# Performance work log

Hardware: AMD Instinct MI355X
Metric: run time of the kernel (lower is better)

The kernel has to match this reference:

```python
import jax, jax.numpy as jnp
import numpy as np

B, C, H, W, IC = 8, 128, 64, 32, 64
NEG = -9.0e15  # matches torch's -9000000000000000.0 mask value


def setup_inputs() -> dict:
    key = jax.random.key(0)
    ks = jax.random.split(key, 8)
    x = jax.random.normal(ks[0], (B, C, H, W), dtype=jnp.float32)
    adj = jax.random.randint(ks[1], (H * W, H * W), 0, 2, dtype=jnp.int32)
    s = 0.1  # keep pre-softmax logits in a sane range
    g_w = jax.random.normal(ks[2], (IC, C), dtype=jnp.float32) * s
    theta_w = jax.random.normal(ks[3], (IC, C), dtype=jnp.float32) * s
    phi_w = jax.random.normal(ks[4], (IC, C), dtype=jnp.float32) * s
    cp_w = jax.random.normal(ks[5], (2 * IC,), dtype=jnp.float32) * s
    g_b = jnp.zeros((IC,), jnp.float32)
    theta_b = jnp.zeros((IC,), jnp.float32)
    phi_b = jnp.zeros((IC,), jnp.float32)
    return {"x": x, "adj": adj, "g_w": g_w, "g_b": g_b, "theta_w": theta_w,
            "theta_b": theta_b, "phi_w": phi_w, "phi_b": phi_b, "cp_w": cp_w}


def reference(x, adj, g_w, g_b, theta_w, theta_b, phi_w, phi_b, cp_w):
    b, c, h, w = x.shape
    n = h * w
    ic = g_w.shape[0]
    xf = x.reshape(b, c, n)  # flatten spatial sites: (B,C,N)
    # 1x1 convs == per-site linear projections
    g_x = jnp.einsum('oc,bcn->bno', g_w, xf) + g_b          # (B,N,IC)
    th = jnp.einsum('oc,bcn->bon', theta_w, xf) + theta_b[:, None]  # (B,IC,N)
    ph = jnp.einsum('oc,bcn->bon', phi_w, xf) + phi_b[:, None]      # (B,IC,N)
    # concat_project 1x1 conv on [theta;phi] channels == broadcast sum of two dot products
    w_t, w_p = cp_w[:ic], cp_w[ic:]
    f_t = jnp.einsum('o,bon->bn', w_t, th)  # (B,N)
    f_p = jnp.einsum('o,bon->bn', w_p, ph)  # (B,N)
    e = jax.nn.leaky_relu(f_t[:, :, None] + f_p[:, None, :], 0.2)  # (B,N,N)
    attention = jnp.where(adj > 0, jnp.float32(NEG), e)
    attention = jax.nn.softmax(attention, axis=-1)
    y = jnp.einsum('bij,bjo->bio', attention, g_x)  # (B,N,IC)
    return y.transpose(0, 2, 1).reshape(b, ic, h, w)
```

## Files before the change

### kernel.cpp

```cpp
#include <hip/hip_runtime.h>
#include <hip/hip_bf16.h>
#include <cstdint>

#define B_   8
#define C_   128
#define IC_  64
#define N_   2048
#define NEGF (-9000000000000000.0f)
#define ROWS 16

typedef __attribute__((ext_vector_type(8))) short bf16x8;
typedef __attribute__((ext_vector_type(4))) float f32x4;

#define OFF_FT   0
#define OFF_FP   16384
#define OFF_VT   32768
#define OFF_VP   32896
#define OFF_VB   33024
#define OFF_GXB  33040

static __device__ __forceinline__ ushort f2bf(float f) {
  __hip_bfloat16 h = __float2bfloat16(f);
  return *reinterpret_cast<ushort*>(&h);
}

__global__ void k_prep(const float* __restrict__ theta_w,
                       const float* __restrict__ theta_b,
                       const float* __restrict__ phi_w,
                       const float* __restrict__ phi_b,
                       const float* __restrict__ cp_w,
                       float* __restrict__ ws) {
  int c = threadIdx.x;
  if (c < C_) {
    float at = 0.f, ap = 0.f;
    for (int o = 0; o < IC_; ++o) {
      at += cp_w[o]       * theta_w[o * C_ + c];
      ap += cp_w[IC_ + o] * phi_w[o * C_ + c];
    }
    ws[OFF_VT + c] = at;
    ws[OFF_VP + c] = ap;
  }
  if (c == 0) {
    float bt = 0.f;
    for (int o = 0; o < IC_; ++o) bt += cp_w[o] * theta_b[o];
    ws[OFF_VB + 0] = bt;
  }
  if (c == 1) {
    float bp = 0.f;
    for (int o = 0; o < IC_; ++o) bp += cp_w[IC_ + o] * phi_b[o];
    ws[OFF_VB + 1] = bp;
  }
}

__global__ __launch_bounds__(256) void k_gx(const float* __restrict__ x,
                                            const float* __restrict__ g_w,
                                            const float* __restrict__ g_b,
                                            float* __restrict__ ws) {
  __shared__ float xs[C_][64];
  __shared__ float wgT[C_][IC_];
  int bx = blockIdx.x;
  int b = bx >> 5, tile = bx & 31;
  int n0 = tile * 64;
  int t = threadIdx.x;

  const float* xb = x + (size_t)b * C_ * N_ + n0;
  for (int idx = t; idx < C_ * 64; idx += 256) {
    int c = idx >> 6, n = idx & 63;
    xs[c][n] = xb[(size_t)c * N_ + n];
  }
  for (int idx = t; idx < C_ * IC_; idx += 256) {
    int c = idx >> 6, o = idx & 63;
    wgT[c][o] = g_w[o * C_ + c];
  }
  __syncthreads();

  int o4 = (t & 15) * 4, n4 = (t >> 4) * 4;
  float acc[4][4] = {};
#pragma unroll 4
  for (int c = 0; c < C_; ++c) {
    float4 xv = *(const float4*)&xs[c][n4];
    float4 wv = *(const float4*)&wgT[c][o4];
    acc[0][0] += wv.x * xv.x; acc[0][1] += wv.x * xv.y; acc[0][2] += wv.x * xv.z; acc[0][3] += wv.x * xv.w;
    acc[1][0] += wv.y * xv.x; acc[1][1] += wv.y * xv.y; acc[1][2] += wv.y * xv.z; acc[1][3] += wv.y * xv.w;
    acc[2][0] += wv.z * xv.x; acc[2][1] += wv.z * xv.y; acc[2][2] += wv.z * xv.z; acc[2][3] += wv.z * xv.w;
    acc[3][0] += wv.w * xv.x; acc[3][1] += wv.w * xv.y; acc[3][2] += wv.w * xv.z; acc[3][3] += wv.w * xv.w;
  }
  __hip_bfloat16* gxT = (__hip_bfloat16*)(ws + OFF_GXB) + (size_t)b * IC_ * N_;
#pragma unroll
  for (int oo = 0; oo < 4; ++oo) {
    float gb = g_b[o4 + oo];
    ushort4 pk = make_ushort4(f2bf(acc[oo][0] + gb), f2bf(acc[oo][1] + gb),
                              f2bf(acc[oo][2] + gb), f2bf(acc[oo][3] + gb));
    *(ushort4*)(gxT + (size_t)(o4 + oo) * N_ + n0 + n4) = pk;
  }

  if (t < 128) {
    int n = t & 63;
    int isp = (t >= 64);
    const float* v = ws + (isp ? OFF_VP : OFF_VT);
    float f = ws[OFF_VB + isp];
    for (int c = 0; c < C_; ++c) f += xs[c][n] * v[c];
    ws[(isp ? OFF_FP : OFF_FT) + b * N_ + n0 + n] = f;
  }
}

__global__ __launch_bounds__(256) void k_attn(const int* __restrict__ adj,
                                              const float* __restrict__ ws,
                                              float* __restrict__ out) {
  __shared__ char smem[ROWS * N_ * 2];
  __shared__ float rowsum[ROWS];

  int bx = blockIdx.x;
  int b = bx >> 7, tile = bx & 127;
  int i0 = tile * ROWS;
  int t = threadIdx.x;
  int w = t >> 6, lane = t & 63;

  const float* f_t = ws + OFF_FT + b * N_;
  const float4* fp4 = (const float4*)(ws + OFF_FP + b * N_);
  const __hip_bfloat16* gxT = (const __hip_bfloat16*)(ws + OFF_GXB) + (size_t)b * IC_ * N_;

  float4 fp[8];
#pragma unroll
  for (int kk = 0; kk < 8; ++kk) fp[kk] = fp4[lane + 64 * kk];

  for (int rr = 0; rr < 4; ++rr) {
    int r = w * 4 + rr;
    float fti = f_t[i0 + r];
    const int4* arow = (const int4*)(adj + (size_t)(i0 + r) * N_);
    float lsum = 0.f;
#pragma unroll
    for (int kk = 0; kk < 8; ++kk) {
      int4 a = arow[lane + 64 * kk];
      float4 f = fp[kk];
      float sx = fti + f.x; sx = sx > 0.f ? sx : 0.2f * sx; sx = (a.x > 0) ? NEGF : sx;
      float sy = fti + f.y; sy = sy > 0.f ? sy : 0.2f * sy; sy = (a.y > 0) ? NEGF : sy;
      float sz = fti + f.z; sz = sz > 0.f ? sz : 0.2f * sz; sz = (a.z > 0) ? NEGF : sz;
      float sw = fti + f.w; sw = sw > 0.f ? sw : 0.2f * sw; sw = (a.w > 0) ? NEGF : sw;
      float px = __expf(sx), py = __expf(sy), pz = __expf(sz), pw = __expf(sw);
      lsum += (px + py) + (pz + pw);
      ushort4 pk = make_ushort4(f2bf(px), f2bf(py), f2bf(pz), f2bf(pw));
      size_t byte = (size_t)r * 4096 + (size_t)lane * 8 + (size_t)kk * 512;
      byte ^= (size_t)((r & 7) << 4);
      *(ushort4*)(smem + byte) = pk;
    }
#pragma unroll
    for (int off = 32; off; off >>= 1) lsum += __shfl_xor(lsum, off, 64);
    if (lane == 0) rowsum[r] = lsum;
  }
  __syncthreads();

  f32x4 acc[4];
#pragma unroll
  for (int ot = 0; ot < 4; ++ot) acc[ot] = (f32x4){0.f, 0.f, 0.f, 0.f};
  int arw = lane & 15, agrp = lane >> 4;
  size_t abase = (size_t)arw * 4096 + (size_t)agrp * 16;
  size_t axor = (size_t)((arw & 7) << 4);
  const __hip_bfloat16* gbase = gxT + (size_t)(lane & 15) * N_ + agrp * 8;

  int kw0 = w * 512;
#pragma unroll
  for (int ks = 0; ks < 16; ++ks) {
    int kb = kw0 + ks * 32;
    bf16x8 af = *(const bf16x8*)(smem + ((abase + (size_t)kb * 2) ^ axor));
    const __hip_bfloat16* gp = gbase + kb;
    bf16x8 b0 = *(const bf16x8*)(gp);
    bf16x8 b1 = *(const bf16x8*)(gp + 16 * N_);
    bf16x8 b2 = *(const bf16x8*)(gp + 32 * N_);
    bf16x8 b3 = *(const bf16x8*)(gp + 48 * N_);
    acc[0] = __builtin_amdgcn_mfma_f32_16x16x32_bf16(af, b0, acc[0], 0, 0, 0);
    acc[1] = __builtin_amdgcn_mfma_f32_16x16x32_bf16(af, b1, acc[1], 0, 0, 0);
    acc[2] = __builtin_amdgcn_mfma_f32_16x16x32_bf16(af, b2, acc[2], 0, 0, 0);
    acc[3] = __builtin_amdgcn_mfma_f32_16x16x32_bf16(af, b3, acc[3], 0, 0, 0);
  }
  __syncthreads();

  float* red = (float*)smem;
#pragma unroll
  for (int ot = 0; ot < 4; ++ot) {
#pragma unroll
    for (int q = 0; q < 4; ++q) {
      int i = agrp * 4 + q;
      int o = ot * 16 + (lane & 15);
      red[(w * 16 + i) * 65 + o] = acc[ot][q];
    }
  }
  __syncthreads();

  int i = t & 15, o0 = t >> 4;
  float inv = 1.f / rowsum[i];
  float* op = out + (size_t)b * IC_ * N_ + i0 + i;
#pragma unroll
  for (int q = 0; q < 4; ++q) {
    int o = o0 + 16 * q;
    float v = red[(0  + i) * 65 + o] + red[(16 + i) * 65 + o]
            + red[(32 + i) * 65 + o] + red[(48 + i) * 65 + o];
    op[(size_t)o * N_] = v * inv;
  }
}

extern "C" void kernel_launch(void* const* d_in, const int* in_sizes, int n_in,
                              void* d_out, int out_size, void* d_ws, size_t ws_size,
                              hipStream_t stream) {
  const float* x       = (const float*)d_in[0];
  const int*   adj     = (const int*)  d_in[1];
  const float* g_w     = (const float*)d_in[2];
  const float* g_b     = (const float*)d_in[3];
  const float* theta_w = (const float*)d_in[4];
  const float* theta_b = (const float*)d_in[5];
  const float* phi_w   = (const float*)d_in[6];
  const float* phi_b   = (const float*)d_in[7];
  const float* cp_w    = (const float*)d_in[8];
  float* out = (float*)d_out;
  float* ws  = (float*)d_ws;

  k_prep<<<1, 128, 0, stream>>>(theta_w, theta_b, phi_w, phi_b, cp_w, ws);
  k_gx<<<B_ * (N_ / 64), 256, 0, stream>>>(x, g_w, g_b, ws);
  k_attn<<<B_ * (N_ / ROWS), 256, 0, stream>>>(adj, ws, out);
}
```

Baseline: 141.6 us.

## Fuse prep into gx, chunk attention over keys and split MFMA by output channels

Removes the separate prep kernel by having every k_gx block recompute the collapsed theta/phi projection vectors, and parallelises the f_t/f_p reduction across all threads. k_attn now walks the key dimension in four 512-wide chunks with double-buffered shared memory, so the staging buffer shrinks and occupancy can rise. Each wave owns 16 output channels across all keys rather than a quarter of the keys for all channels, which removes the cross-wave shared-memory reduction. The softmax uses exp2 with log2e folded into the weights and masks by zeroing instead of exp of a huge negative; the trade-off is one sync per chunk and redundant weight math in each k_gx block.

Result: faster. 133.6 us (-5.6%).

```diff
diff --git a/kernel.cpp b/kernel.cpp
--- a/kernel.cpp
+++ b/kernel.cpp
@@ -2,65 +2,41 @@
 #include <hip/hip_bf16.h>
 #include <cstdint>
 
-#define B_   8
-#define C_   128
-#define IC_  64
-#define N_   2048
-#define NEGF (-9000000000000000.0f)
-#define ROWS 16
+#define B_    8
+#define C_    128
+#define IC_   64
+#define N_    2048
+#define ROWS  16
+#define LOG2E 1.44269504088896340736f
 
 typedef __attribute__((ext_vector_type(8))) short bf16x8;
 typedef __attribute__((ext_vector_type(4))) float f32x4;
 
 #define OFF_FT   0
 #define OFF_FP   16384
-#define OFF_VT   32768
-#define OFF_VP   32896
-#define OFF_VB   33024
-#define OFF_GXB  33040
+#define OFF_GXB  32768
 
 static __device__ __forceinline__ ushort f2bf(float f) {
   __hip_bfloat16 h = __float2bfloat16(f);
   return *reinterpret_cast<ushort*>(&h);
 }
 
-__global__ void k_prep(const float* __restrict__ theta_w,
-                       const float* __restrict__ theta_b,
-                       const float* __restrict__ phi_w,
-                       const float* __restrict__ phi_b,
-                       const float* __restrict__ cp_w,
-                       float* __restrict__ ws) {
-  int c = threadIdx.x;
-  if (c < C_) {
-    float at = 0.f, ap = 0.f;
-    for (int o = 0; o < IC_; ++o) {
-      at += cp_w[o]       * theta_w[o * C_ + c];
-      ap += cp_w[IC_ + o] * phi_w[o * C_ + c];
-    }
-    ws[OFF_VT + c] = at;
-    ws[OFF_VP + c] = ap;
-  }
-  if (c == 0) {
-    float bt = 0.f;
-    for (int o = 0; o < IC_; ++o) bt += cp_w[o] * theta_b[o];
-    ws[OFF_VB + 0] = bt;
-  }
-  if (c == 1) {
-    float bp = 0.f;
-    for (int o = 0; o < IC_; ++o) bp += cp_w[IC_ + o] * phi_b[o];
-    ws[OFF_VB + 1] = bp;
-  }
-}
-
 __global__ __launch_bounds__(256) void k_gx(const float* __restrict__ x,
                                             const float* __restrict__ g_w,
                                             const float* __restrict__ g_b,
+                                            const float* __restrict__ theta_w,
+                                            const float* __restrict__ theta_b,
+                                            const float* __restrict__ phi_w,
+                                            const float* __restrict__ phi_b,
+                                            const float* __restrict__ cp_w,
                                             float* __restrict__ ws) {
   __shared__ float xs[C_][64];
   __shared__ float wgT[C_][IC_];
+  __shared__ float vtp[2][C_];
+  __shared__ float fred[2][4][64];
+  __shared__ float fb[2];
   int bx = blockIdx.x;
-  int b = bx >> 5, tile = bx & 31;
-  int n0 = tile * 64;
+  int b = bx >> 5, n0 = (bx & 31) * 64;
   int t = threadIdx.x;
 
   const float* xb = x + (size_t)b * C_ * N_ + n0;
@@ -71,6 +47,23 @@
   for (int idx = t; idx < C_ * IC_; idx += 256) {
     int c = idx >> 6, o = idx & 63;
     wgT[c][o] = g_w[o * C_ + c];
+  }
+  {
+    int half = t >> 7;
+    int c = t & 127;
+    const float* wmat = half ? phi_w : theta_w;
+    const float* cw = cp_w + half * IC_;
+    float a = 0.f;
+#pragma unroll 8
+    for (int o = 0; o < IC_; ++o) a += cw[o] * wmat[o * C_ + c];
+    vtp[half][c] = a * LOG2E;
+  }
+  if (t < 2) {
+    const float* bv = t ? phi_b : theta_b;
+    const float* cw = cp_w + t * IC_;
+    float a = 0.f;
+    for (int o = 0; o < IC_; ++o) a += cw[o] * bv[o];
+    fb[t] = a * LOG2E;
   }
   __syncthreads();
 
@@ -94,12 +87,24 @@
     *(ushort4*)(gxT + (size_t)(o4 + oo) * N_ + n0 + n4) = pk;
   }
 
+  {
+    int n = t & 63, qr = t >> 6;
+    float ft = 0.f, fp = 0.f;
+#pragma unroll 8
+    for (int cc = 0; cc < 32; ++cc) {
+      int c = qr * 32 + cc;
+      float xv = xs[c][n];
+      ft += xv * vtp[0][c];
+      fp += xv * vtp[1][c];
+    }
+    fred[0][qr][n] = ft;
+    fred[1][qr][n] = fp;
+  }
+  __syncthreads();
   if (t < 128) {
-    int n = t & 63;
-    int isp = (t >= 64);
-    const float* v = ws + (isp ? OFF_VP : OFF_VT);
-    float f = ws[OFF_VB + isp];
-    for (int c = 0; c < C_; ++c) f += xs[c][n] * v[c];
+    int n = t & 63, isp = t >> 6;
+    float f = fb[isp] + fred[isp][0][n] + fred[isp][1][n]
+            + fred[isp][2][n] + fred[isp][3][n];
     ws[(isp ? OFF_FP : OFF_FT) + b * N_ + n0 + n] = f;
   }
 }
@@ -107,7 +112,7 @@
 __global__ __launch_bounds__(256) void k_attn(const int* __restrict__ adj,
                                               const float* __restrict__ ws,
                                               float* __restrict__ out) {
-  __shared__ char smem[ROWS * N_ * 2];
+  __shared__ char pbuf[2][ROWS * 512 * 2];
   __shared__ float rowsum[ROWS];
 
   int bx = blockIdx.x;
@@ -115,88 +120,81 @@
   int i0 = tile * ROWS;
   int t = threadIdx.x;
   int w = t >> 6, lane = t & 63;
+  int c16 = lane & 15, agrp = lane >> 4;
 
   const float* f_t = ws + OFF_FT + b * N_;
   const float4* fp4 = (const float4*)(ws + OFF_FP + b * N_);
   const __hip_bfloat16* gxT = (const __hip_bfloat16*)(ws + OFF_GXB) + (size_t)b * IC_ * N_;
-
-  float4 fp[8];
-#pragma unroll
-  for (int kk = 0; kk < 8; ++kk) fp[kk] = fp4[lane + 64 * kk];
-
+  const __hip_bfloat16* gwav = gxT + (size_t)(w * 16 + c16) * N_ + agrp * 8;
+
+  float fti[4];
+#pragma unroll
+  for (int rr = 0; rr < 4; ++rr) fti[rr] = f_t[i0 + w * 4 + rr];
+
+  float rs[4] = {0.f, 0.f, 0.f, 0.f};
+  f32x4 acc = {0.f, 0.f, 0.f, 0.f};
+
+  for (int ch = 0; ch < 4; ++ch) {
+    int j0 = ch * 512;
+    char* pb = pbuf[ch & 1];
+    float4 fa = fp4[j0 / 4 + lane * 2];
+    float4 fbv = fp4[j0 / 4 + lane * 2 + 1];
+#pragma unroll
+    for (int rr = 0; rr < 4; ++rr) {
+      int r = w * 4 + rr;
+      const int4* ap = (const int4*)(adj + (size_t)(i0 + r) * N_ + j0) + lane * 2;
+      int4 a0 = ap[0], a1 = ap[1];
+      float ft = fti[rr];
+      float s0 = ft + fa.x;  s0 = fmaxf(s0, 0.2f * s0);
+      float s1 = ft + fa.y;  s1 = fmaxf(s1, 0.2f * s1);
+      float s2 = ft + fa.z;  s2 = fmaxf(s2, 0.2f * s2);
+      float s3 = ft + fa.w;  s3 = fmaxf(s3, 0.2f * s3);
+      float s4 = ft + fbv.x; s4 = fmaxf(s4, 0.2f * s4);
+      float s5 = ft + fbv.y; s5 = fmaxf(s5, 0.2f * s5);
+      float s6 = ft + fbv.z; s6 = fmaxf(s6, 0.2f * s6);
+      float s7 = ft + fbv.w; s7 = fmaxf(s7, 0.2f * s7);
+      float p0 = (a0.x > 0) ? 0.f : exp2f(s0);
+      float p1 = (a0.y > 0) ? 0.f : exp2f(s1);
+      float p2 = (a0.z > 0) ? 0.f : exp2f(s2);
+      float p3 = (a0.w > 0) ? 0.f : exp2f(s3);
+      float p4 = (a1.x > 0) ? 0.f : exp2f(s4);
+      float p5 = (a1.y > 0) ? 0.f : exp2f(s5);
+      float p6 = (a1.z > 0) ? 0.f : exp2f(s6);
+      float p7 = (a1.w > 0) ? 0.f : exp2f(s7);
+      rs[rr] += ((p0 + p1) + (p2 + p3)) + ((p4 + p5) + (p6 + p7));
+      bf16x8 pk;
+      pk[0] = (short)f2bf(p0); pk[1] = (short)f2bf(p1);
+      pk[2] = (short)f2bf(p2); pk[3] = (short)f2bf(p3);
+      pk[4] = (short)f2bf(p4); pk[5] = (short)f2bf(p5);
+      pk[6] = (short)f2bf(p6); pk[7] = (short)f2bf(p7);
+      size_t byte = ((size_t)r * 1024 + (size_t)lane * 16) ^ ((size_t)(r & 7) << 4);
+      *(bf16x8*)(pb + byte) = pk;
+    }
+    __syncthreads();
+#pragma unroll
+    for (int ks = 0; ks < 16; ++ks) {
+      size_t ab = ((size_t)c16 * 1024 + (size_t)ks * 64 + (size_t)agrp * 16)
+                ^ ((size_t)(c16 & 7) << 4);
+      bf16x8 af = *(const bf16x8*)(pb + ab);
+      bf16x8 bf = *(const bf16x8*)(gwav + j0 + ks * 32);
+      acc = __builtin_amdgcn_mfma_f32_16x16x32_bf16(af, bf, acc, 0, 0, 0);
+    }
+  }
+
+#pragma unroll
   for (int rr = 0; rr < 4; ++rr) {
-    int r = w * 4 + rr;
-    float fti = f_t[i0 + r];
-    const int4* arow = (const int4*)(adj + (size_t)(i0 + r) * N_);
-    float lsum = 0.f;
-#pragma unroll
-    for (int kk = 0; kk < 8; ++kk) {
-      int4 a = arow[lane + 64 * kk];
-      float4 f = fp[kk];
-      float sx = fti + f.x; sx = sx > 0.f ? sx : 0.2f * sx; sx = (a.x > 0) ? NEGF : sx;
-      float sy = fti + f.y; sy = sy > 0.f ? sy : 0.2f * sy; sy = (a.y > 0) ? NEGF : sy;
-      float sz = fti + f.z; sz = sz > 0.f ? sz : 0.2f * sz; sz = (a.z > 0) ? NEGF : sz;
-      float sw = fti + f.w; sw = sw > 0.f ? sw : 0.2f * sw; sw = (a.w > 0) ? NEGF : sw;
-      float px = __expf(sx), py = __expf(sy), pz = __expf(sz), pw = __expf(sw);
-      lsum += (px + py) + (pz + pw);
-      ushort4 pk = make_ushort4(f2bf(px), f2bf(py), f2bf(pz), f2bf(pw));
-      size_t byte = (size_t)r * 4096 + (size_t)lane * 8 + (size_t)kk * 512;
-      byte ^= (size_t)((r & 7) << 4);
-      *(ushort4*)(smem + byte) = pk;
-    }
-#pragma unroll
-    for (int off = 32; off; off >>= 1) lsum += __shfl_xor(lsum, off, 64);
-    if (lane == 0) rowsum[r] = lsum;
+    float s = rs[rr];
+#pragma unroll
+    for (int off = 32; off; off >>= 1) s += __shfl_xor(s, off, 64);
+    if (lane == 0) rowsum[w * 4 + rr] = s;
   }
   __syncthreads();
 
-  f32x4 acc[4];
-#pragma unroll
-  for (int ot = 0; ot < 4; ++ot) acc[ot] = (f32x4){0.f, 0.f, 0.f, 0.f};
-  int arw = lane & 15, agrp = lane >> 4;
-  size_t abase = (size_t)arw * 4096 + (size_t)agrp * 16;
-  size_t axor = (size_t)((arw & 7) << 4);
-  const __hip_bfloat16* gbase = gxT + (size_t)(lane & 15) * N_ + agrp * 8;
-
-  int kw0 = w * 512;
-#pragma unroll
-  for (int ks = 0; ks < 16; ++ks) {
-    int kb = kw0 + ks * 32;
-    bf16x8 af = *(const bf16x8*)(smem + ((abase + (size_t)kb * 2) ^ axor));
-    const __hip_bfloat16* gp = gbase + kb;
-    bf16x8 b0 = *(const bf16x8*)(gp);
-    bf16x8 b1 = *(const bf16x8*)(gp + 16 * N_);
-    bf16x8 b2 = *(const bf16x8*)(gp + 32 * N_);
-    bf16x8 b3 = *(const bf16x8*)(gp + 48 * N_);
-    acc[0] = __builtin_amdgcn_mfma_f32_16x16x32_bf16(af, b0, acc[0], 0, 0, 0);
-    acc[1] = __builtin_amdgcn_mfma_f32_16x16x32_bf16(af, b1, acc[1], 0, 0, 0);
-    acc[2] = __builtin_amdgcn_mfma_f32_16x16x32_bf16(af, b2, acc[2], 0, 0, 0);
-    acc[3] = __builtin_amdgcn_mfma_f32_16x16x32_bf16(af, b3, acc[3], 0, 0, 0);
-  }
-  __syncthreads();
-
-  float* red = (float*)smem;
-#pragma unroll
-  for (int ot = 0; ot < 4; ++ot) {
-#pragma unroll
-    for (int q = 0; q < 4; ++q) {
-      int i = agrp * 4 + q;
-      int o = ot * 16 + (lane & 15);
-      red[(w * 16 + i) * 65 + o] = acc[ot][q];
-    }
-  }
-  __syncthreads();
-
-  int i = t & 15, o0 = t >> 4;
-  float inv = 1.f / rowsum[i];
-  float* op = out + (size_t)b * IC_ * N_ + i0 + i;
-#pragma unroll
-  for (int q = 0; q < 4; ++q) {
-    int o = o0 + 16 * q;
-    float v = red[(0  + i) * 65 + o] + red[(16 + i) * 65 + o]
-            + red[(32 + i) * 65 + o] + red[(48 + i) * 65 + o];
-    op[(size_t)o * N_] = v * inv;
-  }
+  float4 rsv = *(const float4*)&rowsum[agrp * 4];
+  float* op = out + ((size_t)b * IC_ + w * 16 + c16) * N_ + i0 + agrp * 4;
+  float4 res = make_float4(acc[0] / rsv.x, acc[1] / rsv.y,
+                           acc[2] / rsv.z, acc[3] / rsv.w);
+  *(float4*)op = res;
 }
 
 extern "C" void kernel_launch(void* const* d_in, const int* in_sizes, int n_in,
@@ -214,7 +212,7 @@
   float* out = (float*)d_out;
   float* ws  = (float*)d_ws;
 
-  k_prep<<<1, 128, 0, stream>>>(theta_w, theta_b, phi_w, phi_b, cp_w, ws);
-  k_gx<<<B_ * (N_ / 64), 256, 0, stream>>>(x, g_w, g_b, ws);
+  k_gx<<<B_ * (N_ / 64), 256, 0, stream>>>(x, g_w, g_b, theta_w, theta_b,
+                                           phi_w, phi_b, cp_w, ws);
   k_attn<<<B_ * (N_ / ROWS), 256, 0, stream>>>(adj, ws, out);
 }
```
